# Kernel optimization log

Hardware: AMD Instinct MI355X
Metric: run time of the kernel (lower is better)

Reference implementation:

```python
import jax, jax.numpy as jnp
import numpy as np

B, S, D, H = 2, 4096, 1024, 16
DH = D // H  # 64


def setup_inputs() -> dict:
    key = jax.random.key(0)
    ks = jax.random.split(key, 5)
    x = jax.random.normal(ks[0], (B, S, D), dtype=jnp.float32)
    scale = 1.0 / np.sqrt(D)
    Wq = jax.random.normal(ks[1], (D, D), dtype=jnp.float32) * scale
    Wk = jax.random.normal(ks[2], (D, D), dtype=jnp.float32) * scale
    Wv = jax.random.normal(ks[3], (D, D), dtype=jnp.float32) * scale
    Wo = jax.random.normal(ks[4], (D, D), dtype=jnp.float32) * scale
    bo = jnp.zeros((D,), dtype=jnp.float32)
    return {"x": x, "Wq": Wq, "Wk": Wk, "Wv": Wv, "Wo": Wo, "bo": bo}


def reference(x, Wq, Wk, Wv, Wo, bo):
    b, s, d = x.shape
    # QKV projections (no bias), split heads: [b, s, H, DH]
    q = (x @ Wq).reshape(b, s, H, DH)
    k = (x @ Wk).reshape(b, s, H, DH)
    v = (x @ Wv).reshape(b, s, H, DH)
    # scores: [b, H, s, s]
    scores = jnp.einsum("bqhd,bkhd->bhqk", q, k)
    # causal mask: upper triangle (j > i) set to -inf, then scale by sqrt(d_head)
    causal = jnp.triu(jnp.ones((s, s), dtype=bool), k=1)
    scores = jnp.where(causal, -jnp.inf, scores)
    weights = jax.nn.softmax(scores / jnp.sqrt(jnp.float32(DH)), axis=-1)
    # dropout rate is 0.0 -> identity
    ctx = jnp.einsum("bhqk,bkhd->bqhd", weights, v).reshape(b, s, d)
    return ctx @ Wo + bo
```

## Files before the change

kernel.cpp:

```cpp
#include <hip/hip_runtime.h>
#include <hip/hip_bf16.h>
#include <stdint.h>
#include <math.h>

#define BATCH 2
#define S_LEN 4096
#define DMODEL 1024
#define NH 16
#define DHEAD 64
#define MTOK (BATCH * S_LEN)

#define QSCALE 0.1803368801111793f

typedef unsigned short u16;
typedef __attribute__((ext_vector_type(8))) short bf16x8;
typedef __attribute__((ext_vector_type(4))) float f32x4;
typedef __attribute__((ext_vector_type(16))) float f32x16;
typedef __attribute__((ext_vector_type(4))) unsigned short u16x4;

__device__ __forceinline__ float b2f(u16 u) {
  union { unsigned int i; float f; } v; v.i = ((unsigned int)u) << 16; return v.f;
}
__device__ __forceinline__ u16 f2b(float f) {
  union { float f; unsigned int i; } v; v.f = f;
  unsigned int r = v.i + 0x7FFF + ((v.i >> 16) & 1);
  return (u16)(r >> 16);
}
__device__ __forceinline__ unsigned int pk2(float hi, float lo) {
  union { float f; unsigned int u; } a, b; a.f = hi; b.f = lo;
  return __builtin_amdgcn_perm(a.u, b.u, 0x07060302u);
}
__device__ __forceinline__ void pswap(unsigned int& a, unsigned int& b) {
  asm("v_permlane32_swap_b32 %0, %1" : "+v"(a), "+v"(b));
}

__device__ __forceinline__ void gl_lds16(const u16* g, u16* l) {
  __builtin_amdgcn_global_load_lds(
      (__attribute__((address_space(1))) void*)(u16*)g,
      (__attribute__((address_space(3))) void*)l, 16, 0, 0);
}

__global__ void detect_dtype(const unsigned int* __restrict__ x, int* __restrict__ flag) {
  __shared__ int cnt;
  if (threadIdx.x == 0) cnt = 0;
  __syncthreads();
  int c = 0;
  for (int i = threadIdx.x; i < 4096; i += 256) {
    unsigned int w = x[i];
    int e = (w >> 7) & 0xFF;
    if (e >= 100 && e <= 135) c++;
  }
  atomicAdd(&cnt, c);
  __syncthreads();
  if (threadIdx.x == 0) *flag = (cnt > 2048) ? 1 : 0;
}

__global__ void convert_x(const void* __restrict__ xin, u16* __restrict__ xc,
                          const int* __restrict__ flagp) {
  const int isb = *flagp;
  long e = ((long)blockIdx.x * 256 + threadIdx.x) * 4;
  if (isb) {
    *(uint2*)&xc[e] = *(const uint2*)((const u16*)xin + e);
  } else {
    float4 f = *(const float4*)((const float*)xin + e);
    xc[e + 0] = f2b(f.x);
    xc[e + 1] = f2b(f.y);
    xc[e + 2] = f2b(f.z);
    xc[e + 3] = f2b(f.w);
  }
}

__global__ void transpose4(const void* __restrict__ W0, const void* __restrict__ W1,
                           const void* __restrict__ W2, const void* __restrict__ W3,
                           u16* __restrict__ out, const int* __restrict__ flagp) {
  __shared__ u16 tile[32][33];
  const int isb = *flagp;
  int z = blockIdx.z;
  const void* W = (z == 0) ? W0 : (z == 1) ? W1 : (z == 2) ? W2 : W3;
  u16* o = out + (long)z * (DMODEL * DMODEL);
  int x = blockIdx.x * 32 + threadIdx.x;
  int y0 = blockIdx.y * 32;
  if (isb) {
    const u16* Wb = (const u16*)W;
#pragma unroll
    for (int i = 0; i < 32; i += 8)
      tile[threadIdx.y + i][threadIdx.x] = Wb[(long)(y0 + threadIdx.y + i) * DMODEL + x];
  } else {
    const float* Wf = (const float*)W;
#pragma unroll
    for (int i = 0; i < 32; i += 8)
      tile[threadIdx.y + i][threadIdx.x] = f2b(Wf[(long)(y0 + threadIdx.y + i) * DMODEL + x]);
  }
  __syncthreads();
  int x2 = blockIdx.y * 32 + threadIdx.x;
  int y2 = blockIdx.x * 32;
#pragma unroll
  for (int i = 0; i < 32; i += 8)
    o[(long)(y2 + threadIdx.y + i) * DMODEL + x2] = tile[threadIdx.x][threadIdx.y + i];
}

#define BM2 256
#define BN2 128
#define BK2 32
#define NT2 (DMODEL / BK2)

#define VM3 asm volatile("s_waitcnt vmcnt(3)" ::: "memory")
#define VM0 asm volatile("s_waitcnt vmcnt(0)" ::: "memory")
#define BARX do { asm volatile("" ::: "memory"); __builtin_amdgcn_s_barrier(); \
                  asm volatile("" ::: "memory"); } while (0)

#define GEMM_CORE2(A_, Bt_)                                                       \
  __shared__ __align__(16) u16 lds[2 * 12288];                                    \
  const int tid = threadIdx.x;                                                    \
  const int w = tid >> 6;                                                         \
  const int lane = tid & 63;                                                      \
  const int m0 = blockIdx.y * BM2;                                                \
  const int n0 = blockIdx.x * BN2;                                                \
  const int wm = (w >> 1) * 64;                                                   \
  const int wn = (w & 1) * 64;                                                    \
  const int lc = lane & 15;                                                       \
  const int lq = lane >> 4;                                                       \
  const u16* pA = (A_) + (long)(m0 + w * 16 + (lane >> 2)) * DMODEL + (lane & 3) * 8; \
  const u16* pB = (Bt_) + (long)(n0 + w * 16 + (lane >> 2)) * DMODEL + (lane & 3) * 8; \
  u16* aB0 = lds + w * 512;                                                       \
  u16* bB0 = lds + 8192 + w * 512;                                                \
  f32x4 acc[4][4] = {};                                                           \
  gl_lds16(pA, aB0);                                                              \
  gl_lds16(pA + 128 * DMODEL, aB0 + 4096);                                        \
  gl_lds16(pB, bB0);                                                              \
  gl_lds16(pA + BK2, aB0 + 12288);                                                \
  gl_lds16(pA + BK2 + 128 * DMODEL, aB0 + 4096 + 12288);                          \
  gl_lds16(pB + BK2, bB0 + 12288);                                                \
  for (int t = 0; t < NT2; ++t) {                                                 \
    if (t < NT2 - 1) { VM3; } else { VM0; }                                       \
    BARX;                                                                         \
    const u16* la = lds + (t & 1) * 12288;                                        \
    const u16* lb = la + 8192;                                                    \
    bf16x8 af[4], bg[4];                                                          \
    _Pragma("unroll")                                                             \
    for (int i = 0; i < 4; ++i)                                                   \
      af[i] = *(const bf16x8*)&la[(wm + i * 16 + lc) * 32 + lq * 8];              \
    _Pragma("unroll")                                                             \
    for (int j = 0; j < 4; ++j)                                                   \
      bg[j] = *(const bf16x8*)&lb[(wn + j * 16 + lc) * 32 + lq * 8];              \
    _Pragma("unroll")                                                             \
    for (int i = 0; i < 4; ++i)                                                   \
      _Pragma("unroll")                                                           \
      for (int j = 0; j < 4; ++j)                                                 \
        acc[i][j] = __builtin_amdgcn_mfma_f32_16x16x32_bf16(af[i], bg[j], acc[i][j], 0, 0, 0); \
    BARX;                                                                         \
    if (t + 2 < NT2) {                                                            \
      const u16* at = pA + (t + 2) * BK2;                                         \
      const u16* bt = pB + (t + 2) * BK2;                                         \
      u16* ad = aB0 + (t & 1) * 12288;                                            \
      u16* bd = bB0 + (t & 1) * 12288;                                            \
      gl_lds16(at, ad);                                                           \
      gl_lds16(at + 128 * DMODEL, ad + 4096);                                     \
      gl_lds16(bt, bd);                                                           \
    }                                                                             \
  }

__global__ __launch_bounds__(512, 1)
void gemm_qkv(const u16* __restrict__ A, const u16* __restrict__ Bt,
              u16* __restrict__ Qo, u16* __restrict__ Ko, u16* __restrict__ Vo) {
  GEMM_CORE2(A, Bt)
#pragma unroll
  for (int i = 0; i < 4; ++i) {
#pragma unroll
    for (int j = 0; j < 4; ++j) {
      int n = n0 + wn + j * 16 + lc;
      int rgn = n >> 10;
      int nn = n & 1023;
      int h = nn >> 6, dh = nn & (DHEAD - 1);
      int m_base = m0 + wm + i * 16 + lq * 4;
      int b = m_base >> 12, s0q = m_base & (S_LEN - 1);
      if (rgn == 2) {
        long idx_v = (((long)(b * NH + h)) * DHEAD + dh) * S_LEN + s0q;
        u16x4 vv;
#pragma unroll
        for (int r = 0; r < 4; ++r) vv[r] = f2b(acc[i][j][r]);
        *(u16x4*)&Vo[idx_v] = vv;
      } else {
        float sc = (rgn == 0) ? QSCALE : 1.0f;
        u16* dst = (rgn == 0) ? Qo : Ko;
#pragma unroll
        for (int r = 0; r < 4; ++r) {
          long idx_r = (((long)(b * NH + h)) * S_LEN + s0q + r) * DHEAD + dh;
          dst[idx_r] = f2b(acc[i][j][r] * sc);
        }
      }
    }
  }
}

__global__ __launch_bounds__(512, 1)
void gemm_out(const u16* __restrict__ A, const u16* __restrict__ Bt,
              const void* __restrict__ bias, void* __restrict__ C,
              const int* __restrict__ flagp) {
  GEMM_CORE2(A, Bt)
  const int isb = *flagp;
#pragma unroll
  for (int i = 0; i < 4; ++i) {
#pragma unroll
    for (int j = 0; j < 4; ++j) {
      int n = n0 + wn + j * 16 + lc;
      float bv = isb ? b2f(((const u16*)bias)[n]) : ((const float*)bias)[n];
#pragma unroll
      for (int r = 0; r < 4; ++r) {
        int m = m0 + wm + i * 16 + lq * 4 + r;
        float v = acc[i][j][r] + bv;
        if (isb) ((u16*)C)[(long)m * DMODEL + n] = f2b(v);
        else     ((float*)C)[(long)m * DMODEL + n] = v;
      }
    }
  }
}

__global__ __launch_bounds__(256, 2)
void flash_attn(const u16* __restrict__ Q, const u16* __restrict__ K,
                const u16* __restrict__ Vt, u16* __restrict__ ctx) {
  __shared__ __align__(16) u16 lK[64 * 64];
  __shared__ __align__(16) u16 lV[64 * 64];

  const int tid = threadIdx.x;
  const int w = tid >> 6;
  const int lane = tid & 63;
  const int l31 = lane & 31;
  const int l5 = lane >> 5;

  const int hb = blockIdx.x;
  const int h = hb & (NH - 1);
  const int b = hb >> 4;
  const int qt = gridDim.y - 1 - (int)blockIdx.y;
  const int q0 = qt * 128;

  const int bh = b * NH + h;
  const u16* Qb = Q + (long)bh * S_LEN * DHEAD;
  const u16* Kb = K + (long)bh * S_LEN * DHEAD;
  const u16* Vb = Vt + (long)bh * DHEAD * S_LEN;

  const int qa = q0 + w * 32;
  const int myq = qa + l31;

  bf16x8 aq[4];
#pragma unroll
  for (int c = 0; c < 4; ++c)
    aq[c] = *(const bf16x8*)(Qb + (long)myq * DHEAD + c * 16 + l5 * 8);

  union OU { unsigned int wd[4]; bf16x8 v; } ones;
#pragma unroll
  for (int i = 0; i < 4; ++i) ones.wd[i] = 0x3F803F80u;

  const int srow = tid >> 2;
  const int sc0 = (tid & 3) * 2;
  const int sd0 = srow * 64 + ((sc0 ^ (srow & 7)) * 8);
  const int sd1 = srow * 64 + (((sc0 + 1) ^ (srow & 7)) * 8);
  const u16* kp = Kb + (long)srow * DHEAD + sc0 * 8;
  const u16* vp = Vb + (long)srow * S_LEN + sc0 * 8;

  const int kmax = q0 + 64;
  bf16x8 kr0 = *(const bf16x8*)kp;
  bf16x8 kr1 = *(const bf16x8*)(kp + 8);
  bf16x8 vr0 = *(const bf16x8*)vp;
  bf16x8 vr1 = *(const bf16x8*)(vp + 8);
  const u16* kpre = kp + 64 * DHEAD;
  const u16* vpre = vp + 64;

  f32x16 o0 = {}, o1 = {};
  f32x16 lacc = {};
  const int xsw = l31 & 7;

  int offK[4][2], offV[4][2];
#pragma unroll
  for (int c = 0; c < 4; ++c) {
    const int ch = c * 2 + l5;
    offK[c][0] = l31 * 64 + ((ch ^ xsw) * 8);
    offK[c][1] = (32 + l31) * 64 + ((ch ^ xsw) * 8);
    offV[c][0] = offK[c][0];
    offV[c][1] = offK[c][1];
  }

  for (int k0 = 0; k0 <= kmax; k0 += 64) {
    *(bf16x8*)&lK[sd0] = kr0;
    *(bf16x8*)&lK[sd1] = kr1;
    *(bf16x8*)&lV[sd0] = vr0;
    *(bf16x8*)&lV[sd1] = vr1;
    __syncthreads();

    if (k0 + 64 <= kmax) {
      kr0 = *(const bf16x8*)kpre;
      kr1 = *(const bf16x8*)(kpre + 8);
      vr0 = *(const bf16x8*)vpre;
      vr1 = *(const bf16x8*)(vpre + 8);
      kpre += 64 * DHEAD;
      vpre += 64;
    }

    if (k0 <= qa + 31) {
      f32x16 s0 = {}, s1 = {};
      __builtin_amdgcn_s_setprio(1);
#pragma unroll
      for (int c = 0; c < 4; ++c) {
        bf16x8 ak0 = *(const bf16x8*)&lK[offK[c][0]];
        bf16x8 ak1 = *(const bf16x8*)&lK[offK[c][1]];
        s0 = __builtin_amdgcn_mfma_f32_32x32x16_bf16(ak0, aq[c], s0, 0, 0, 0);
        s1 = __builtin_amdgcn_mfma_f32_32x32x16_bf16(ak1, aq[c], s1, 0, 0, 0);
      }
      __builtin_amdgcn_s_setprio(0);

      const bool masked = (k0 + 63 > qa);
      union BPU { unsigned int wd[4]; bf16x8 v; };
      BPU bp[4];
#pragma unroll
      for (int ph = 0; ph < 2; ++ph) {
        const f32x16 sv = ph ? s1 : s0;
        float p[16];
#pragma unroll
        for (int rr = 0; rr < 16; ++rr) {
          float e = __builtin_amdgcn_exp2f(sv[rr]);
          if (masked) {
            int kv = k0 + ph * 32 + (rr & 3) + 8 * (rr >> 2) + 4 * l5;
            e = (kv > myq) ? 0.0f : e;
          }
          p[rr] = e;
        }
#pragma unroll
        for (int g = 0; g < 2; ++g) {
          unsigned int A0 = pk2(p[8 * g + 1], p[8 * g + 0]);
          unsigned int A1 = pk2(p[8 * g + 3], p[8 * g + 2]);
          unsigned int B0 = pk2(p[8 * g + 5], p[8 * g + 4]);
          unsigned int B1 = pk2(p[8 * g + 7], p[8 * g + 6]);
          pswap(A0, B0);
          pswap(A1, B1);
          const int kc = ph * 2 + g;
          bp[kc].wd[0] = A0; bp[kc].wd[1] = A1;
          bp[kc].wd[2] = B0; bp[kc].wd[3] = B1;
        }
      }

      __builtin_amdgcn_s_setprio(1);
#pragma unroll
      for (int kc = 0; kc < 4; ++kc) {
        bf16x8 av0 = *(const bf16x8*)&lV[offV[kc][0]];
        bf16x8 av1 = *(const bf16x8*)&lV[offV[kc][1]];
        o0 = __builtin_amdgcn_mfma_f32_32x32x16_bf16(av0, bp[kc].v, o0, 0, 0, 0);
        o1 = __builtin_amdgcn_mfma_f32_32x32x16_bf16(av1, bp[kc].v, o1, 0, 0, 0);
        lacc = __builtin_amdgcn_mfma_f32_32x32x16_bf16(ones.v, bp[kc].v, lacc, 0, 0, 0);
      }
      __builtin_amdgcn_s_setprio(0);
    }
    __syncthreads();
  }

  float inv = 1.0f / lacc[0];

  u16* cp = ctx + ((long)(b * S_LEN + myq)) * DMODEL + h * DHEAD;
#pragma unroll
  for (int d32 = 0; d32 < 2; ++d32) {
    const f32x16 ov = d32 ? o1 : o0;
#pragma unroll
    for (int g = 0; g < 4; ++g) {
      u16x4 st;
#pragma unroll
      for (int r = 0; r < 4; ++r) st[r] = f2b(ov[4 * g + r] * inv);
      *(u16x4*)&cp[d32 * 32 + g * 8 + l5 * 4] = st;
    }
  }
}

extern "C" void kernel_launch(void* const* d_in, const int* in_sizes, int n_in,
                              void* d_out, int out_size, void* d_ws, size_t ws_size,
                              hipStream_t stream) {
  const void* x  = d_in[0];
  const void* Wq = d_in[1];
  const void* Wk = d_in[2];
  const void* Wv = d_in[3];
  const void* Wo = d_in[4];
  const void* bo = d_in[5];
  u16* ws = (u16*)d_ws;

  u16* wt  = ws;
  u16* wto = wt + 3145728;
  u16* Qb  = ws + 4194304;
  u16* Vtb = ws + 12582912;
  u16* xc  = ws + 20971520;
  u16* ctx = xc;
  int* flag = (int*)(ws + 29360128);
  u16* Kb  = (u16*)d_out;

  detect_dtype<<<1, 256, 0, stream>>>((const unsigned int*)x, flag);
  convert_x<<<8192, 256, 0, stream>>>(x, xc, flag);
  transpose4<<<dim3(32, 32, 4), dim3(32, 8), 0, stream>>>(Wq, Wk, Wv, Wo, wt, flag);

  gemm_qkv<<<dim3(3 * DMODEL / BN2, MTOK / BM2), 512, 0, stream>>>(xc, wt, Qb, Kb, Vtb);

  flash_attn<<<dim3(NH * BATCH, S_LEN / 128), 256, 0, stream>>>(Qb, Kb, Vtb, ctx);

  gemm_out<<<dim3(DMODEL / BN2, MTOK / BM2), 512, 0, stream>>>(ctx, wto, bo, d_out, flag);
}
```

Measured before the change: 294.1 us.

## Retile projection GEMMs to 128x256 blocks with 4 waves, 8x4 MFMA tiles

Both projection GEMMs move from 256x128 tiles with 8 waves (each wave 64x64) to 128x256 tiles with 4 waves, each wave owning a full 128-row by 64-column strip. Each wave now reads every A row and its own B columns from LDS, holding 32 accumulators, and launch bounds allow two blocks per CU. The aim is more MFMA work per LDS fragment load and better latency hiding through two resident blocks. The cost is higher register pressure per wave and a different global load pattern, with six async loads per stage and a matching vmcnt wait.

```diff
diff --git a/kernel.cpp b/kernel.cpp
--- a/kernel.cpp
+++ b/kernel.cpp
@@ -99,80 +99,80 @@
     o[(long)(y2 + threadIdx.y + i) * DMODEL + x2] = tile[threadIdx.x][threadIdx.y + i];
 }
 
-#define BM2 256
-#define BN2 128
-#define BK2 32
-#define NT2 (DMODEL / BK2)
-
-#define VM3 asm volatile("s_waitcnt vmcnt(3)" ::: "memory")
+#define BM3 128
+#define BN3 256
+#define BK3 32
+#define NT3 (DMODEL / BK3)
+#define BUF3 12288
+
+#define VM6 asm volatile("s_waitcnt vmcnt(6)" ::: "memory")
 #define VM0 asm volatile("s_waitcnt vmcnt(0)" ::: "memory")
 #define BARX do { asm volatile("" ::: "memory"); __builtin_amdgcn_s_barrier(); \
                   asm volatile("" ::: "memory"); } while (0)
 
-#define GEMM_CORE2(A_, Bt_)                                                       \
-  __shared__ __align__(16) u16 lds[2 * 12288];                                    \
+#define STAGE3(t_, dst_)                                                          \
+  do {                                                                            \
+    const u16* a_ = pA + (t_) * BK3;                                              \
+    const u16* b_ = pB + (t_) * BK3;                                              \
+    u16* ad_ = (dst_) + w * 1024;                                                 \
+    u16* bd_ = (dst_) + 4096 + w * 2048;                                          \
+    gl_lds16(a_, ad_);                                                            \
+    gl_lds16(a_ + 16 * DMODEL, ad_ + 512);                                        \
+    gl_lds16(b_, bd_);                                                            \
+    gl_lds16(b_ + 16 * DMODEL, bd_ + 512);                                        \
+    gl_lds16(b_ + 32 * DMODEL, bd_ + 1024);                                       \
+    gl_lds16(b_ + 48 * DMODEL, bd_ + 1536);                                       \
+  } while (0)
+
+#define GEMM_CORE3(A_, Bt_)                                                       \
+  __shared__ __align__(16) u16 lds[2 * BUF3];                                     \
   const int tid = threadIdx.x;                                                    \
   const int w = tid >> 6;                                                         \
   const int lane = tid & 63;                                                      \
-  const int m0 = blockIdx.y * BM2;                                                \
-  const int n0 = blockIdx.x * BN2;                                                \
-  const int wm = (w >> 1) * 64;                                                   \
-  const int wn = (w & 1) * 64;                                                    \
+  const int m0 = blockIdx.y * BM3;                                                \
+  const int n0 = blockIdx.x * BN3;                                                \
+  const int wn = w * 64;                                                          \
   const int lc = lane & 15;                                                       \
   const int lq = lane >> 4;                                                       \
-  const u16* pA = (A_) + (long)(m0 + w * 16 + (lane >> 2)) * DMODEL + (lane & 3) * 8; \
-  const u16* pB = (Bt_) + (long)(n0 + w * 16 + (lane >> 2)) * DMODEL + (lane & 3) * 8; \
-  u16* aB0 = lds + w * 512;                                                       \
-  u16* bB0 = lds + 8192 + w * 512;                                                \
-  f32x4 acc[4][4] = {};                                                           \
-  gl_lds16(pA, aB0);                                                              \
-  gl_lds16(pA + 128 * DMODEL, aB0 + 4096);                                        \
-  gl_lds16(pB, bB0);                                                              \
-  gl_lds16(pA + BK2, aB0 + 12288);                                                \
-  gl_lds16(pA + BK2 + 128 * DMODEL, aB0 + 4096 + 12288);                          \
-  gl_lds16(pB + BK2, bB0 + 12288);                                                \
-  for (int t = 0; t < NT2; ++t) {                                                 \
-    if (t < NT2 - 1) { VM3; } else { VM0; }                                       \
+  const u16* pA = (A_) + (long)(m0 + w * 32 + (lane >> 2)) * DMODEL + (lane & 3) * 8; \
+  const u16* pB = (Bt_) + (long)(n0 + w * 64 + (lane >> 2)) * DMODEL + (lane & 3) * 8; \
+  f32x4 acc[8][4] = {};                                                           \
+  STAGE3(0, lds);                                                                 \
+  STAGE3(1, lds + BUF3);                                                          \
+  for (int t = 0; t < NT3; ++t) {                                                 \
+    if (t < NT3 - 1) { VM6; } else { VM0; }                                       \
     BARX;                                                                         \
-    const u16* la = lds + (t & 1) * 12288;                                        \
-    const u16* lb = la + 8192;                                                    \
-    bf16x8 af[4], bg[4];                                                          \
-    _Pragma("unroll")                                                             \
-    for (int i = 0; i < 4; ++i)                                                   \
-      af[i] = *(const bf16x8*)&la[(wm + i * 16 + lc) * 32 + lq * 8];              \
+    const u16* la = lds + (t & 1) * BUF3;                                         \
+    const u16* lb = la + 4096;                                                    \
+    bf16x8 af[8], bg[4];                                                          \
     _Pragma("unroll")                                                             \
     for (int j = 0; j < 4; ++j)                                                   \
       bg[j] = *(const bf16x8*)&lb[(wn + j * 16 + lc) * 32 + lq * 8];              \
     _Pragma("unroll")                                                             \
-    for (int i = 0; i < 4; ++i)                                                   \
+    for (int i = 0; i < 8; ++i)                                                   \
+      af[i] = *(const bf16x8*)&la[(i * 16 + lc) * 32 + lq * 8];                   \
+    _Pragma("unroll")                                                             \
+    for (int i = 0; i < 8; ++i)                                                   \
       _Pragma("unroll")                                                           \
       for (int j = 0; j < 4; ++j)                                                 \
         acc[i][j] = __builtin_amdgcn_mfma_f32_16x16x32_bf16(af[i], bg[j], acc[i][j], 0, 0, 0); \
     BARX;                                                                         \
-    if (t + 2 < NT2) {                                                            \
-      const u16* at = pA + (t + 2) * BK2;                                         \
-      const u16* bt = pB + (t + 2) * BK2;                                         \
-      u16* ad = aB0 + (t & 1) * 12288;                                            \
-      u16* bd = bB0 + (t & 1) * 12288;                                            \
-      gl_lds16(at, ad);                                                           \
-      gl_lds16(at + 128 * DMODEL, ad + 4096);                                     \
-      gl_lds16(bt, bd);                                                           \
-    }                                                                             \
-  }
-
-__global__ __launch_bounds__(512, 1)
+    if (t + 2 < NT3) { STAGE3(t + 2, lds + (t & 1) * BUF3); }                     \
+  }
+
+__global__ __launch_bounds__(256, 2)
 void gemm_qkv(const u16* __restrict__ A, const u16* __restrict__ Bt,
               u16* __restrict__ Qo, u16* __restrict__ Ko, u16* __restrict__ Vo) {
-  GEMM_CORE2(A, Bt)
-#pragma unroll
-  for (int i = 0; i < 4; ++i) {
+  GEMM_CORE3(A, Bt)
+#pragma unroll
+  for (int i = 0; i < 8; ++i) {
 #pragma unroll
     for (int j = 0; j < 4; ++j) {
       int n = n0 + wn + j * 16 + lc;
       int rgn = n >> 10;
       int nn = n & 1023;
       int h = nn >> 6, dh = nn & (DHEAD - 1);
-      int m_base = m0 + wm + i * 16 + lq * 4;
+      int m_base = m0 + i * 16 + lq * 4;
       int b = m_base >> 12, s0q = m_base & (S_LEN - 1);
       if (rgn == 2) {
         long idx_v = (((long)(b * NH + h)) * DHEAD + dh) * S_LEN + s0q;
@@ -193,21 +193,21 @@
   }
 }
 
-__global__ __launch_bounds__(512, 1)
+__global__ __launch_bounds__(256, 2)
 void gemm_out(const u16* __restrict__ A, const u16* __restrict__ Bt,
               const void* __restrict__ bias, void* __restrict__ C,
               const int* __restrict__ flagp) {
-  GEMM_CORE2(A, Bt)
+  GEMM_CORE3(A, Bt)
   const int isb = *flagp;
 #pragma unroll
-  for (int i = 0; i < 4; ++i) {
+  for (int i = 0; i < 8; ++i) {
 #pragma unroll
     for (int j = 0; j < 4; ++j) {
       int n = n0 + wn + j * 16 + lc;
       float bv = isb ? b2f(((const u16*)bias)[n]) : ((const float*)bias)[n];
 #pragma unroll
       for (int r = 0; r < 4; ++r) {
-        int m = m0 + wm + i * 16 + lq * 4 + r;
+        int m = m0 + i * 16 + lq * 4 + r;
         float v = acc[i][j][r] + bv;
         if (isb) ((u16*)C)[(long)m * DMODEL + n] = f2b(v);
         else     ((float*)C)[(long)m * DMODEL + n] = v;
@@ -392,9 +392,9 @@
   convert_x<<<8192, 256, 0, stream>>>(x, xc, flag);
   transpose4<<<dim3(32, 32, 4), dim3(32, 8), 0, stream>>>(Wq, Wk, Wv, Wo, wt, flag);
 
-  gemm_qkv<<<dim3(3 * DMODEL / BN2, MTOK / BM2), 512, 0, stream>>>(xc, wt, Qb, Kb, Vtb);
+  gemm_qkv<<<dim3(3 * DMODEL / BN3, MTOK / BM3), 256, 0, stream>>>(xc, wt, Qb, Kb, Vtb);
 
   flash_attn<<<dim3(NH * BATCH, S_LEN / 128), 256, 0, stream>>>(Qb, Kb, Vtb, ctx);
 
-  gemm_out<<<dim3(DMODEL / BN2, MTOK / BM2), 512, 0, stream>>>(ctx, wto, bo, d_out, flag);
-}
+  gemm_out<<<dim3(DMODEL / BN3, MTOK / BM3), 256, 0, stream>>>(ctx, wto, bo, d_out, flag);
+}
```

Measured after the change: 288.9 us. No clear change (-1.7%).
